# Performance work log

Hardware: AMD Instinct MI355X
Metric: run time of the kernel (lower is better)

Reference implementation:

```python
import jax, jax.numpy as jnp
import numpy as np

HEAD_NUM = 16

def setup_inputs() -> dict:
    key = jax.random.key(0)
    kq, kk, kv = jax.random.split(key, 3)
    shape = (4, 2048, 1024)  # [B, N, C]
    return {
        "query_layer": jax.random.normal(kq, shape, dtype=jnp.float32),
        "key_layer": jax.random.normal(kk, shape, dtype=jnp.float32),
        "value_layer": jax.random.normal(kv, shape, dtype=jnp.float32),
    }

def _split_heads(x, h):
    B, N, C = x.shape
    return x.reshape(B, N, h, C // h).transpose(0, 2, 1, 3)  # [B,H,N,d]

def reference(query_layer, key_layer, value_layer):
    B, N, C = query_layer.shape
    h = HEAD_NUM
    d = C // h
    q = _split_heads(query_layer, h)
    k = _split_heads(key_layer, h)
    v = _split_heads(value_layer, h)
    scores = jnp.einsum('bhnd,bhmd->bhnm', q, k) / jnp.sqrt(jnp.asarray(d, q.dtype))
    probs = jax.nn.softmax(scores, axis=-1)
    ctx = jnp.einsum('bhnm,bhmd->bhnd', probs, v)
    return ctx.transpose(0, 2, 1, 3).reshape(B, N, C)
```

## Files before the change

### kernel.cpp

```cpp
#include <hip/hip_runtime.h>
#include <hip/hip_bf16.h>

#define B_   4
#define N_   2048
#define C_   1024
#define NT   32
#define QSCALE 0.18033688011112042f

typedef __attribute__((ext_vector_type(8)))  short short8;
typedef __attribute__((ext_vector_type(4)))  float f32x4;
typedef __attribute__((ext_vector_type(16))) float f32x16;
typedef __attribute__((ext_vector_type(2)))  int   int2v;

__device__ __forceinline__ unsigned short f2bf(float x) {
    union { __hip_bfloat16 h; unsigned short u; } c;
    c.h = __float2bfloat16(x);
    return c.u;
}
__device__ __forceinline__ float fast_exp2(float x) {
    float r; asm("v_exp_f32 %0, %1" : "=v"(r) : "v"(x)); return r;
}
__device__ __forceinline__ int cvtpk(float a, float b) {
    int r; asm("v_cvt_pk_bf16_f32 %0, %1, %2" : "=v"(r) : "v"(a), "v"(b)); return r;
}

__global__ __launch_bounds__(256) void prepack(
    const float* __restrict__ K, const float* __restrict__ V,
    unsigned short* __restrict__ Kt, unsigned short* __restrict__ Vt)
{
    __shared__ __align__(16) unsigned short kl[4096];
    __shared__ __align__(16) unsigned short vl[4096];
    const int L = blockIdx.x;
    const int xcd = L & 7;
    const int j = L >> 3;
    const int head = xcd + 8 * (j >> 5);
    const int t = j & 31;
    const int b = head >> 4, h = head & 15;
    const int tid = threadIdx.x;
    const int r = tid >> 2, cb = tid & 3;
    const size_t head_off = (size_t)b * N_ * C_ + (size_t)h * 64;
    const int kv0 = t * 64;
    const int blk_out = head * NT + t;

    {
        const float* src = K + head_off + (size_t)(kv0 + r) * C_ + cb * 16;
        f32x4 x0 = *(const f32x4*)(src);
        f32x4 x1 = *(const f32x4*)(src + 4);
        f32x4 x2 = *(const f32x4*)(src + 8);
        f32x4 x3 = *(const f32x4*)(src + 12);
        short8 p0, p1;
        #pragma unroll
        for (int i = 0; i < 4; ++i) {
            p0[i] = (short)f2bf(x0[i]); p0[i + 4] = (short)f2bf(x1[i]);
            p1[i] = (short)f2bf(x2[i]); p1[i + 4] = (short)f2bf(x3[i]);
        }
        const int swz = (r & 7) << 3;
        *(short8*)&kl[r * 64 + ((cb * 16) ^ swz)]     = p0;
        *(short8*)&kl[r * 64 + ((cb * 16 + 8) ^ swz)] = p1;
    }
    {
        const float* src = V + head_off + (size_t)(kv0 + r) * C_ + cb * 16;
        f32x4 y0 = *(const f32x4*)(src);
        f32x4 y1 = *(const f32x4*)(src + 4);
        f32x4 y2 = *(const f32x4*)(src + 8);
        f32x4 y3 = *(const f32x4*)(src + 12);
        #pragma unroll
        for (int i = 0; i < 4; ++i) {
            int d0 = cb * 16 + i;
            vl[d0 * 64 + (r ^ ((d0 & 7) << 3))] = f2bf(y0[i]);
            int d1 = cb * 16 + 4 + i;
            vl[d1 * 64 + (r ^ ((d1 & 7) << 3))] = f2bf(y1[i]);
            int d2 = cb * 16 + 8 + i;
            vl[d2 * 64 + (r ^ ((d2 & 7) << 3))] = f2bf(y2[i]);
            int d3 = cb * 16 + 12 + i;
            vl[d3 * 64 + (r ^ ((d3 & 7) << 3))] = f2bf(y3[i]);
        }
    }
    __syncthreads();
    #pragma unroll
    for (int cc = 0; cc < 2; ++cc) {
        const int c  = tid + cc * 256;
        const int f  = c >> 6;
        const int ln = c & 63;
        const int row = (f & 1) * 32 + (ln & 31);
        const int col = (f >> 1) * 16 + (ln >> 5) * 8;
        const int sw  = (row & 7) << 3;
        short8 kk = *(const short8*)&kl[row * 64 + (col ^ sw)];
        short8 vv = *(const short8*)&vl[row * 64 + (col ^ sw)];
        *(short8*)&Kt[(size_t)blk_out * 4096 + c * 8] = kk;
        *(short8*)&Vt[(size_t)blk_out * 4096 + c * 8] = vv;
    }
}

#define MFMA32(A, B, C) __builtin_amdgcn_mfma_f32_32x32x16_bf16((A), (B), (C), 0, 0, 0)

#define TILE_BODY(T, PO0, PO1, PO2, PO3, PI0, PI1, PI2, PI3, FIRST)            \
{                                                                              \
    if ((T) == 0) { asm volatile("s_waitcnt vmcnt(0)" ::: "memory"); }         \
    else          { asm volatile("s_waitcnt vmcnt(8)" ::: "memory"); }         \
    __builtin_amdgcn_s_barrier();                                              \
    if ((T) + 1 < NT) stageK((T) + 1, cur ^ 1);                                \
    const unsigned short* kl = &klds[cur][0];                                  \
    f32x16 s0, s1;                                                             \
    {                                                                          \
        const float nm = (FIRST) ? 0.0f : -m_r;   \
        _Pragma("unroll")                                                      \
        for (int r = 0; r < 16; ++r) { s0[r] = nm; s1[r] = nm; }               \
    }                                                                          \
    __builtin_amdgcn_s_setprio(1);                                             \
    {                                                                          \
        short8 kf0 = *(const short8*)&kl[0 * 1024 + lofs];                     \
        short8 kf1 = *(const short8*)&kl[0 * 1024 + 512 + lofs];               \
        s0 = MFMA32(kf0, qfrag[0], s0);                                        \
        s1 = MFMA32(kf1, qfrag[0], s1);                                        \
        kf0 = *(const short8*)&kl[1 * 1024 + lofs];                            \
        kf1 = *(const short8*)&kl[1 * 1024 + 512 + lofs];                      \
        s0 = MFMA32(kf0, qfrag[1], s0);                                        \
        s1 = MFMA32(kf1, qfrag[1], s1);                                        \
        kf0 = *(const short8*)&kl[2 * 1024 + lofs];                            \
        kf1 = *(const short8*)&kl[2 * 1024 + 512 + lofs];                      \
        s0 = MFMA32(kf0, qfrag[2], s0);                                        \
        s1 = MFMA32(kf1, qfrag[2], s1);                                        \
        kf0 = *(const short8*)&kl[3 * 1024 + lofs];                            \
        kf1 = *(const short8*)&kl[3 * 1024 + 512 + lofs];                      \
        s0 = MFMA32(kf0, qfrag[3], s0);                                        \
        s1 = MFMA32(kf1, qfrag[3], s1);                                        \
    }                                                                          \
    if (!(FIRST)) {      \
        o0 = MFMA32(vr0, PI0, o0);  o1 = MFMA32(vr1, PI0, o1);                 \
        o0 = MFMA32(vr2, PI1, o0);  o1 = MFMA32(vr3, PI1, o1);                 \
        o0 = MFMA32(vr4, PI2, o0);  o1 = MFMA32(vr5, PI2, o1);                 \
        o0 = MFMA32(vr6, PI3, o0);  o1 = MFMA32(vr7, PI3, o1);                 \
    }                                                                          \
    __builtin_amdgcn_s_setprio(0);                                             \
    {                \
        const unsigned short* vtp = vbase + (size_t)(T) * 4096 + lofs;         \
        vr0 = *(const short8*)(vtp);                                           \
        vr1 = *(const short8*)(vtp + 512);                                     \
        vr2 = *(const short8*)(vtp + 1024);                                    \
        vr3 = *(const short8*)(vtp + 1536);                                    \
        vr4 = *(const short8*)(vtp + 2048);                                    \
        vr5 = *(const short8*)(vtp + 2560);                                    \
        vr6 = *(const short8*)(vtp + 3072);                                    \
        vr7 = *(const short8*)(vtp + 3584);                                    \
    }                                                                          \
    float mx[8];                                                               \
    _Pragma("unroll")                                                          \
    for (int r = 0; r < 8; ++r)                                                \
        mx[r] = fmaxf(fmaxf(s0[r], s0[r + 8]), fmaxf(s1[r], s1[r + 8]));       \
    _Pragma("unroll")                                                          \
    for (int st = 4; st; st >>= 1) {                                           \
        _Pragma("unroll")                                                      \
        for (int r = 0; r < st; ++r) mx[r] = fmaxf(mx[r], mx[r + st]);         \
    }                                                                          \
    int2v msw = __builtin_amdgcn_permlane32_swap(                              \
        __float_as_int(mx[0]), __float_as_int(mx[0]), false, false);           \
    const float rmp = fmaxf(__int_as_float(msw[0]), __int_as_float(msw[1]));   \
    if (FIRST) {                                                               \
        m_r = rmp;                                                             \
        _Pragma("unroll")                                                      \
        for (int r = 0; r < 16; ++r) { s0[r] -= rmp; s1[r] -= rmp; }           \
    } else if (!__all(rmp <= 8.0f)) {             \
        const float d = fmaxf(rmp, 0.0f);                                      \
        const float corr = fast_exp2(-d);                                      \
        m_r += d;                                                              \
        l_half *= corr;                                                        \
        _Pragma("unroll")                                                      \
        for (int r = 0; r < 16; ++r) {                                         \
            s0[r] -= d; s1[r] -= d;                                            \
            o0[r] *= corr; o1[r] *= corr;                                      \
        }                                                                      \
    }                                                                          \
    _Pragma("unroll")                                                          \
    for (int r = 0; r < 16; ++r) {                                             \
        s0[r] = fast_exp2(s0[r]);                                              \
        s1[r] = fast_exp2(s1[r]);                                              \
    }                                                                          \
    {                              \
        int w0, w1, w2, w3; int2v sA, sB;                                      \
        union { int i[4]; short8 v; } u;                                       \
        w0 = cvtpk(s0[0], s0[1]);  w1 = cvtpk(s0[2], s0[3]);                   \
        w2 = cvtpk(s0[4], s0[5]);  w3 = cvtpk(s0[6], s0[7]);                   \
        sA = __builtin_amdgcn_permlane32_swap(w0, w2, false, false);           \
        sB = __builtin_amdgcn_permlane32_swap(w1, w3, false, false);           \
        u.i[0] = sA[0]; u.i[1] = sB[0]; u.i[2] = sA[1]; u.i[3] = sB[1];        \
        PO0 = u.v;                                                             \
        w0 = cvtpk(s0[8], s0[9]);  w1 = cvtpk(s0[10], s0[11]);                 \
        w2 = cvtpk(s0[12], s0[13]); w3 = cvtpk(s0[14], s0[15]);                \
        sA = __builtin_amdgcn_permlane32_swap(w0, w2, false, false);           \
        sB = __builtin_amdgcn_permlane32_swap(w1, w3, false, false);           \
        u.i[0] = sA[0]; u.i[1] = sB[0]; u.i[2] = sA[1]; u.i[3] = sB[1];        \
        PO1 = u.v;                                                             \
        w0 = cvtpk(s1[0], s1[1]);  w1 = cvtpk(s1[2], s1[3]);                   \
        w2 = cvtpk(s1[4], s1[5]);  w3 = cvtpk(s1[6], s1[7]);                   \
        sA = __builtin_amdgcn_permlane32_swap(w0, w2, false, false);           \
        sB = __builtin_amdgcn_permlane32_swap(w1, w3, false, false);           \
        u.i[0] = sA[0]; u.i[1] = sB[0]; u.i[2] = sA[1]; u.i[3] = sB[1];        \
        PO2 = u.v;                                                             \
        w0 = cvtpk(s1[8], s1[9]);  w1 = cvtpk(s1[10], s1[11]);                 \
        w2 = cvtpk(s1[12], s1[13]); w3 = cvtpk(s1[14], s1[15]);                \
        sA = __builtin_amdgcn_permlane32_swap(w0, w2, false, false);           \
        sB = __builtin_amdgcn_permlane32_swap(w1, w3, false, false);           \
        u.i[0] = sA[0]; u.i[1] = sB[0]; u.i[2] = sA[1]; u.i[3] = sB[1];        \
        PO3 = u.v;                                                             \
    }                                                                          \
    float aa[8];                                                               \
    _Pragma("unroll")                                                          \
    for (int r = 0; r < 8; ++r) aa[r] = (s0[r] + s0[r + 8]) + (s1[r] + s1[r + 8]); \
    _Pragma("unroll")                                                          \
    for (int st = 4; st; st >>= 1) {                                           \
        _Pragma("unroll")                                                      \
        for (int r = 0; r < st; ++r) aa[r] += aa[r + st];                      \
    }                                                                          \
    l_half += aa[0];                                                           \
    cur ^= 1;                                                                  \
}

__global__ __launch_bounds__(256, 3) void attn_fwd(
    const float* __restrict__ Q, const unsigned short* __restrict__ Kt,
    const unsigned short* __restrict__ Vt, float* __restrict__ O)
{
    __shared__ __align__(16) unsigned short klds[2][4096];

    const int L = blockIdx.x;
    const int xcd = L & 7;
    const int j = L >> 3;
    const int head = xcd + 8 * (j >> 4);
    const int qt = j & 15;
    const int b = head >> 4, h = head & 15;

    const int tid  = threadIdx.x;
    const int wave = tid >> 6;
    const int lane = tid & 63;
    const int l31  = lane & 31;
    const int hi   = lane >> 5;

    const unsigned short* kbase = Kt + (size_t)head * (NT * 4096);
    const unsigned short* vbase = Vt + (size_t)head * (NT * 4096);
    const float* qp = Q + (size_t)b * N_ * C_ + (size_t)h * 64;
    float*       op = O + (size_t)b * N_ * C_ + (size_t)h * 64;

    const int qrow = qt * 128 + wave * 32 + l31;
    short8 qfrag[4];
    {
        const float* qr = qp + (size_t)qrow * C_ + hi * 8;
        #pragma unroll
        for (int ks = 0; ks < 4; ++ks) {
            f32x4 x0 = *(const f32x4*)(qr + ks * 16);
            f32x4 x1 = *(const f32x4*)(qr + ks * 16 + 4);
            short8 a;
            #pragma unroll
            for (int i = 0; i < 4; ++i) {
                a[i]     = (short)f2bf(x0[i] * QSCALE);
                a[i + 4] = (short)f2bf(x1[i] * QSCALE);
            }
            qfrag[ks] = a;
        }
    }

    f32x16 o0 = {}, o1 = {};
    float m_r = 0.0f, l_half = 0.0f;

    const int lofs = lane * 8;

    auto stageK = [&](int t, int buf) {
        const unsigned short* kg = kbase + (size_t)t * 4096 + wave * 1024 + lofs;
        __builtin_amdgcn_global_load_lds((const __attribute__((address_space(1))) void*)kg,
            (__attribute__((address_space(3))) void*)&klds[buf][wave * 1024], 16, 0, 0);
        __builtin_amdgcn_global_load_lds((const __attribute__((address_space(1))) void*)(kg + 512),
            (__attribute__((address_space(3))) void*)&klds[buf][wave * 1024 + 512], 16, 0, 0);
    };

    int cur = 0;
    short8 pA0, pA1, pA2, pA3, pB0, pB1, pB2, pB3;
    short8 vr0, vr1, vr2, vr3, vr4, vr5, vr6, vr7;

    stageK(0, 0);

    TILE_BODY(0, pA0, pA1, pA2, pA3, pB0, pB1, pB2, pB3, true)
    for (int t = 1; t < NT - 1; t += 2) {
        TILE_BODY(t,     pB0, pB1, pB2, pB3, pA0, pA1, pA2, pA3, false)
        TILE_BODY(t + 1, pA0, pA1, pA2, pA3, pB0, pB1, pB2, pB3, false)
    }
    TILE_BODY(NT - 1, pB0, pB1, pB2, pB3, pA0, pA1, pA2, pA3, false)

    __builtin_amdgcn_s_setprio(1);
    o0 = MFMA32(vr0, pB0, o0);  o1 = MFMA32(vr1, pB0, o1);
    o0 = MFMA32(vr2, pB1, o0);  o1 = MFMA32(vr3, pB1, o1);
    o0 = MFMA32(vr4, pB2, o0);  o1 = MFMA32(vr5, pB2, o1);
    o0 = MFMA32(vr6, pB3, o0);  o1 = MFMA32(vr7, pB3, o1);
    __builtin_amdgcn_s_setprio(0);

    int2v lsw = __builtin_amdgcn_permlane32_swap(
        __float_as_int(l_half), __float_as_int(l_half), false, false);
    const float l_r = __int_as_float(lsw[0]) + __int_as_float(lsw[1]);
    const float inv = 1.0f / l_r;

    float* orow = op + (size_t)qrow * C_;
    #pragma unroll
    for (int bb = 0; bb < 4; ++bb) {
        f32x4 w0, w1;
        #pragma unroll
        for (int i = 0; i < 4; ++i) {
            w0[i] = o0[4 * bb + i] * inv;
            w1[i] = o1[4 * bb + i] * inv;
        }
        *(f32x4*)(orow + 8 * bb + 4 * hi)      = w0;
        *(f32x4*)(orow + 32 + 8 * bb + 4 * hi) = w1;
    }
}

extern "C" void kernel_launch(void* const* d_in, const int* in_sizes, int n_in,
                              void* d_out, int out_size, void* d_ws, size_t ws_size,
                              hipStream_t stream) {
    const float* q = (const float*)d_in[0];
    const float* k = (const float*)d_in[1];
    const float* v = (const float*)d_in[2];
    float* o = (float*)d_out;
    unsigned short* Kt = (unsigned short*)d_ws;
    unsigned short* Vt = Kt + (size_t)64 * NT * 4096;
    prepack<<<dim3(64 * NT), dim3(256), 0, stream>>>(k, v, Kt, Vt);
    attn_fwd<<<dim3(1024), dim3(256), 0, stream>>>(q, Kt, Vt, o);
}
```

Baseline: 111.4 us.

## Split KV sequence across wave pairs within block and merge partial softmax

Each block now handles 64 query rows instead of 128. Its four waves form two query slices by two KV halves, and each wave pair walks only 16 of the 32 KV tiles. At the end the second-half waves write their partial output, running max and partial sum to LDS, and the first-half waves merge them with rescaled exponentials before normalizing. This doubles the grid to 2048 blocks and halves each wave's serial loop length, aiming at more parallelism and a shorter critical path. In exchange K/V data is loaded twice as often per query row, LDS use doubles, and a merge step with extra barriers is added.

After: 135.1 us. +21.2%, slower.

```diff
diff --git a/kernel.cpp b/kernel.cpp
--- a/kernel.cpp
+++ b/kernel.cpp
@@ -5,6 +5,7 @@
 #define N_   2048
 #define C_   1024
 #define NT   32
+#define NTH  16
 #define QSCALE 0.18033688011112042f
 
 typedef __attribute__((ext_vector_type(8)))  short short8;
@@ -99,8 +100,8 @@
     if ((T) == 0) { asm volatile("s_waitcnt vmcnt(0)" ::: "memory"); }         \
     else          { asm volatile("s_waitcnt vmcnt(8)" ::: "memory"); }         \
     __builtin_amdgcn_s_barrier();                                              \
-    if ((T) + 1 < NT) stageK((T) + 1, cur ^ 1);                                \
-    const unsigned short* kl = &klds[cur][0];                                  \
+    if ((T) + 1 < NTH) stageK((T) + 1, cur ^ 1);                               \
+    const unsigned short* kl = &klds[kvhalf][cur][0];                          \
     f32x16 s0, s1;                                                             \
     {                                                                          \
         const float nm = (FIRST) ? 0.0f : -m_r;   \
@@ -134,7 +135,7 @@
     }                                                                          \
     __builtin_amdgcn_s_setprio(0);                                             \
     {                \
-        const unsigned short* vtp = vbase + (size_t)(T) * 4096 + lofs;         \
+        const unsigned short* vtp = kvvbase + (size_t)(T) * 4096 + lofs;       \
         vr0 = *(const short8*)(vtp);                                           \
         vr1 = *(const short8*)(vtp + 512);                                     \
         vr2 = *(const short8*)(vtp + 1024);                                    \
@@ -220,27 +221,29 @@
     const float* __restrict__ Q, const unsigned short* __restrict__ Kt,
     const unsigned short* __restrict__ Vt, float* __restrict__ O)
 {
-    __shared__ __align__(16) unsigned short klds[2][4096];
+    __shared__ __align__(16) unsigned short klds[2][2][4096];
 
     const int L = blockIdx.x;
     const int xcd = L & 7;
     const int j = L >> 3;
-    const int head = xcd + 8 * (j >> 4);
-    const int qt = j & 15;
+    const int head = xcd + 8 * (j >> 5);
+    const int qt = j & 31;
     const int b = head >> 4, h = head & 15;
 
     const int tid  = threadIdx.x;
     const int wave = tid >> 6;
+    const int qslice = wave & 1;
+    const int kvhalf = wave >> 1;
     const int lane = tid & 63;
     const int l31  = lane & 31;
     const int hi   = lane >> 5;
 
-    const unsigned short* kbase = Kt + (size_t)head * (NT * 4096);
-    const unsigned short* vbase = Vt + (size_t)head * (NT * 4096);
+    const unsigned short* kvkbase = Kt + (size_t)head * (NT * 4096) + (size_t)kvhalf * (NTH * 4096);
+    const unsigned short* kvvbase = Vt + (size_t)head * (NT * 4096) + (size_t)kvhalf * (NTH * 4096);
     const float* qp = Q + (size_t)b * N_ * C_ + (size_t)h * 64;
     float*       op = O + (size_t)b * N_ * C_ + (size_t)h * 64;
 
-    const int qrow = qt * 128 + wave * 32 + l31;
+    const int qrow = qt * 64 + qslice * 32 + l31;
     short8 qfrag[4];
     {
         const float* qr = qp + (size_t)qrow * C_ + hi * 8;
@@ -264,11 +267,16 @@
     const int lofs = lane * 8;
 
     auto stageK = [&](int t, int buf) {
-        const unsigned short* kg = kbase + (size_t)t * 4096 + wave * 1024 + lofs;
+        const unsigned short* kg = kvkbase + (size_t)t * 4096 + qslice * 2048 + lofs;
+        unsigned short* kd = &klds[kvhalf][buf][qslice * 2048];
         __builtin_amdgcn_global_load_lds((const __attribute__((address_space(1))) void*)kg,
-            (__attribute__((address_space(3))) void*)&klds[buf][wave * 1024], 16, 0, 0);
+            (__attribute__((address_space(3))) void*)kd, 16, 0, 0);
         __builtin_amdgcn_global_load_lds((const __attribute__((address_space(1))) void*)(kg + 512),
-            (__attribute__((address_space(3))) void*)&klds[buf][wave * 1024 + 512], 16, 0, 0);
+            (__attribute__((address_space(3))) void*)(kd + 512), 16, 0, 0);
+        __builtin_amdgcn_global_load_lds((const __attribute__((address_space(1))) void*)(kg + 1024),
+            (__attribute__((address_space(3))) void*)(kd + 1024), 16, 0, 0);
+        __builtin_amdgcn_global_load_lds((const __attribute__((address_space(1))) void*)(kg + 1536),
+            (__attribute__((address_space(3))) void*)(kd + 1536), 16, 0, 0);
     };
 
     int cur = 0;
@@ -278,11 +286,11 @@
     stageK(0, 0);
 
     TILE_BODY(0, pA0, pA1, pA2, pA3, pB0, pB1, pB2, pB3, true)
-    for (int t = 1; t < NT - 1; t += 2) {
+    for (int t = 1; t < NTH - 1; t += 2) {
         TILE_BODY(t,     pB0, pB1, pB2, pB3, pA0, pA1, pA2, pA3, false)
         TILE_BODY(t + 1, pA0, pA1, pA2, pA3, pB0, pB1, pB2, pB3, false)
     }
-    TILE_BODY(NT - 1, pB0, pB1, pB2, pB3, pA0, pA1, pA2, pA3, false)
+    TILE_BODY(NTH - 1, pB0, pB1, pB2, pB3, pA0, pA1, pA2, pA3, false)
 
     __builtin_amdgcn_s_setprio(1);
     o0 = MFMA32(vr0, pB0, o0);  o1 = MFMA32(vr1, pB0, o1);
@@ -290,6 +298,49 @@
     o0 = MFMA32(vr4, pB2, o0);  o1 = MFMA32(vr5, pB2, o1);
     o0 = MFMA32(vr6, pB3, o0);  o1 = MFMA32(vr7, pB3, o1);
     __builtin_amdgcn_s_setprio(0);
+
+    __syncthreads();
+    float* exch = (float*)&klds[0][0][0];
+    float* slot = exch + (size_t)(qslice * 64 + lane) * 36;
+    if (kvhalf == 1) {
+        #pragma unroll
+        for (int c4 = 0; c4 < 4; ++c4) {
+            f32x4 w;
+            #pragma unroll
+            for (int i = 0; i < 4; ++i) w[i] = o0[c4 * 4 + i];
+            *(f32x4*)(slot + c4 * 4) = w;
+        }
+        #pragma unroll
+        for (int c4 = 0; c4 < 4; ++c4) {
+            f32x4 w;
+            #pragma unroll
+            for (int i = 0; i < 4; ++i) w[i] = o1[c4 * 4 + i];
+            *(f32x4*)(slot + 16 + c4 * 4) = w;
+        }
+        slot[32] = m_r;
+        slot[33] = l_half;
+    }
+    __syncthreads();
+    if (kvhalf == 1) return;
+
+    {
+        const float mB = slot[32];
+        const float lB = slot[33];
+        const float m  = fmaxf(m_r, mB);
+        const float cA = fast_exp2(m_r - m);
+        const float cB = fast_exp2(mB - m);
+        l_half = l_half * cA + lB * cB;
+        #pragma unroll
+        for (int c4 = 0; c4 < 4; ++c4) {
+            f32x4 wb0 = *(const f32x4*)(slot + c4 * 4);
+            f32x4 wb1 = *(const f32x4*)(slot + 16 + c4 * 4);
+            #pragma unroll
+            for (int i = 0; i < 4; ++i) {
+                o0[c4 * 4 + i] = o0[c4 * 4 + i] * cA + wb0[i] * cB;
+                o1[c4 * 4 + i] = o1[c4 * 4 + i] * cA + wb1[i] * cB;
+            }
+        }
+    }
 
     int2v lsw = __builtin_amdgcn_permlane32_swap(
         __float_as_int(l_half), __float_as_int(l_half), false, false);
@@ -320,5 +371,5 @@
     unsigned short* Kt = (unsigned short*)d_ws;
     unsigned short* Vt = Kt + (size_t)64 * NT * 4096;
     prepack<<<dim3(64 * NT), dim3(256), 0, stream>>>(k, v, Kt, Vt);
-    attn_fwd<<<dim3(1024), dim3(256), 0, stream>>>(q, Kt, Vt, o);
-}
+    attn_fwd<<<dim3(2048), dim3(256), 0, stream>>>(q, Kt, Vt, o);
+}
```
